# Kernel optimization log

Hardware: AMD Instinct MI355X
Metric: run time of the kernel (lower is better)

The kernel has to match this reference:

```python
import jax, jax.numpy as jnp
import numpy as np

# Dimensions matching init_kwargs
B, S, D, d_feat, O = 64, 1024, 64, 2, 10
L = S // 2  # label_site
STD = 0.01  # 'random_eye' init noise scale


def setup_inputs() -> dict:
    key = jax.random.key(0)
    k1, k2, k3, k4 = jax.random.split(key, 4)
    x = jax.random.normal(k1, (B, S, d_feat), dtype=jnp.float32)
    # InputRegion tensors, bond_str 'slri': eye over (l, r) broadcast over (s, i)
    W_left = jnp.eye(D, dtype=jnp.float32)[None, :, :, None] \
        + STD * jax.random.normal(k2, (L, D, D, d_feat), dtype=jnp.float32)
    W_right = jnp.eye(D, dtype=jnp.float32)[None, :, :, None] \
        + STD * jax.random.normal(k3, (S - L, D, D, d_feat), dtype=jnp.float32)
    # OutputSite tensor, bond_str 'olr': eye over (l, r) broadcast over o
    out_core = jnp.eye(D, dtype=jnp.float32)[None, :, :] \
        + STD * jax.random.normal(k4, (O, D, D), dtype=jnp.float32)
    return {"x": x, "W_left": W_left, "out_core": out_core, "W_right": W_right}


def reference(x, W_left, out_core, W_right):
    # x: [B, S, d]; W_left: [L, D, D, d]; out_core: [O, D, D]; W_right: [S-L, D, D, d]
    Ls = W_left.shape[0]
    Dv = W_left.shape[1]
    Bv = x.shape[0]
    # Per-site matrices (einsum 'slri,bsi->bslr'), laid out scan-major [S, B, D, D]
    mats_l = jnp.einsum('slri,bsi->sblr', W_left, x[:, :Ls])
    mats_r = jnp.einsum('slri,bsi->sblr', W_right, x[:, Ls:])
    # Open boundary edge vectors e = [1, 0, ..., 0]
    e = jnp.zeros((Dv,), dtype=x.dtype).at[0].set(1.0)
    v0 = jnp.broadcast_to(e, (Bv, Dv))
    # Left-to-right vector propagation through left chain
    def lstep(v, m):
        return jnp.einsum('bl,blr->br', v, m), None
    vL, _ = jax.lax.scan(lstep, v0, mats_l)
    # Right-to-left vector propagation through right chain
    def rstep(w, m):
        return jnp.einsum('blr,br->bl', m, w), None
    wR, _ = jax.lax.scan(rstep, v0, mats_r, reverse=True)
    # Contract through the output core: [B, O]
    return jnp.einsum('bl,olr,br->bo', vL, out_core, wR)
```

## Files before the change

### kernel.cpp

```cpp
#include <hip/hip_runtime.h>
#include <stdint.h>

#define NSITE 512
#define DD    64
#define NB    64
#define NO    10
#define NSEG  16
#define SEGLEN 32
#define SLAB_BYTES 32768
#define PACK_BYTES 16384

typedef short bf16x8 __attribute__((ext_vector_type(8)));
typedef float f32x16 __attribute__((ext_vector_type(16)));

__device__ __forceinline__ uint32_t pk2(float a, float b) {
    return __builtin_amdgcn_perm(__float_as_uint(b), __float_as_uint(a), 0x07060302);
}

__device__ __forceinline__ float2 pkmul2(float2 a, float2 b) {
    float2 r;
    asm("v_pk_mul_f32 %0, %1, %2" : "=v"(r) : "v"(a), "v"(b));
    return r;
}

__global__ __launch_bounds__(256) void pack_kernel(float* __restrict__ wl,
                                                   float* __restrict__ wr) {
    const int g = blockIdx.x;
    const int right = (g >= NSITE) ? 1 : 0;
    const int s = right ? g - NSITE : g;
    float* base = (right ? wr : wl) + (size_t)s * (SLAB_BYTES / 4);

    __shared__ float2 st[DD * 65];
    const float4* src4 = (const float4*)base;
    for (int e4 = threadIdx.x; e4 < DD * DD / 2; e4 += 256) {
        const float4 v = src4[e4];
        const int e = e4 * 2;
        float2* d = &st[(e >> 6) * 65 + (e & 63)];
        d[0] = make_float2(v.x, v.y);
        d[1] = make_float2(v.z, v.w);
    }
    __syncthreads();

    uint32_t* out = (uint32_t*)base;
    #pragma unroll
    for (int rr = 0; rr < 16; ++rr) {
        const int od = rr * 256 + threadIdx.x;
        const int chunk = od >> 8, i = chunk >> 3, sk = chunk & 7;
        const int H = (od >> 7) & 1, m5 = (od >> 2) & 31, d = od & 3;
        const int m = 32 * i + m5, k = 8 * sk + 4 * H + d;
        const float2 a = right ? st[m * 65 + k] : st[k * 65 + m];
        out[od] = pk2(a.x, a.y);
    }
}

__device__ __forceinline__ void dma16(const void* gp, void* lp) {
    __builtin_amdgcn_global_load_lds(
        (const __attribute__((address_space(1))) uint32_t*)gp,
        (__attribute__((address_space(3))) uint32_t*)lp, 16, 0, 0);
}

__global__ __launch_bounds__(256, 2) void stage1_kernel(
        const float* __restrict__ x, float* __restrict__ wl, float* __restrict__ wr) {
    const int bid  = blockIdx.x;
    const int side = bid >> 8;
    const int seg  = (bid >> 4) & 15;
    const int bq   = bid & 15;
    const int wave = threadIdx.x >> 6;
    const int lane = threadIdx.x & 63;
    const int b    = bq * 4 + wave;
    const int m5   = lane & 31;
    const int H    = lane >> 5;

    __shared__ __align__(16) char ring[4][PACK_BYTES];
    __shared__ float2 xs[4][SEGLEN];

    char* wbuf = (char*)(side ? wr : wl);

    if (lane < SEGLEN) {
        const float2* xp = ((const float2*)x) + (size_t)b * 1024 + (side ? NSITE : 0);
        const int sg = seg * SEGLEN + (side ? SEGLEN - 1 - lane : lane);
        xs[wave][lane] = xp[sg];
    }

    auto siteAddr = [&](int t) -> const char* {
        const int sg = seg * SEGLEN + (side ? SEGLEN - 1 - t : t);
        return wbuf + (size_t)sg * SLAB_BYTES;
    };

    #pragma unroll
    for (int t0 = 0; t0 < 2; ++t0) {
        const char* sb = siteAddr(t0);
        #pragma unroll
        for (int c = 0; c < 4; ++c) {
            const int ch = wave * 4 + c;
            dma16(sb + ch * 1024 + lane * 16, ring[t0] + ch * 1024);
        }
    }

    f32x16 acc[2][2];
    #pragma unroll
    for (int i = 0; i < 2; ++i)
        #pragma unroll
        for (int j = 0; j < 2; ++j)
            #pragma unroll
            for (int q = 0; q < 16; ++q) {
                const int row = (q & 3) + 8 * (q >> 2) + 4 * H;
                acc[i][j][q] = (i == j && row == m5) ? 1.f : 0.f;
            }

    f32x16 zf;
    #pragma unroll
    for (int q = 0; q < 16; ++q) zf[q] = 0.f;

    union BU { bf16x8 v; uint32_t w[4]; };

    for (int t = 0; t < SEGLEN; ++t) {
        int t2 = t + 2; if (t2 > SEGLEN - 1) t2 = SEGLEN - 1;
        {
            const char* sb = siteAddr(t2);
            char* lb = ring[(t + 2) & 3];
            #pragma unroll
            for (int c = 0; c < 4; ++c) {
                const int ch = wave * 4 + c;
                dma16(sb + ch * 1024 + lane * 16, lb + ch * 1024);
            }
        }
        asm volatile("s_waitcnt vmcnt(8)" ::: "memory");
        asm volatile("s_barrier" ::: "memory");

        const char* rb = ring[t & 3];
        const float2 xv = xs[wave][t];
        const float2 xx = make_float2(xv.x, xv.x);
        const float2 xy = make_float2(xv.y, xv.y);

        BU bfa[8][2];
        #pragma unroll
        for (int sk = 0; sk < 8; ++sk) {
            const int mi = sk >> 2, qb = 4 * (sk & 3);
            #pragma unroll
            for (int j = 0; j < 2; ++j)
                #pragma unroll
                for (int dp = 0; dp < 2; ++dp) {
                    const float2 v01 = make_float2(acc[mi][j][qb + 2 * dp],
                                                   acc[mi][j][qb + 2 * dp + 1]);
                    const float2 pa = pkmul2(xx, v01);
                    const float2 pb = pkmul2(xy, v01);
                    bfa[sk][j].w[2 * dp + 0] = pk2(pa.x, pb.x);
                    bfa[sk][j].w[2 * dp + 1] = pk2(pa.y, pb.y);
                }
        }

        __builtin_amdgcn_s_setprio(1);
        #pragma unroll
        for (int sk = 0; sk < 8; ++sk) {
            #pragma unroll
            for (int i = 0; i < 2; ++i) {
                union { bf16x8 v; uint4 u; } a;
                a.u = *(const uint4*)(rb + (i * 8 + sk) * 1024 + lane * 16);
                #pragma unroll
                for (int j = 0; j < 2; ++j)
                    acc[i][j] = __builtin_amdgcn_mfma_f32_32x32x16_bf16(
                        a.v, bfa[sk][j].v, (sk == 0) ? zf : acc[i][j], 0, 0, 0);
            }
        }
        __builtin_amdgcn_s_setprio(0);
    }

    {
        const int p = b * NSEG + seg;
        char* pdst = wbuf + (size_t)(p >> 1) * SLAB_BYTES + PACK_BYTES + (p & 1) * 8192;
        #pragma unroll
        for (int i = 0; i < 2; ++i)
            #pragma unroll
            for (int j = 0; j < 2; ++j) {
                const int c = 32 * j + m5;
                #pragma unroll
                for (int Q = 0; Q < 4; ++Q) {
                    const int r0 = 32 * i + 8 * Q + 4 * H;
                    uint2 val;
                    val.x = pk2(acc[i][j][4 * Q + 0], acc[i][j][4 * Q + 1]);
                    val.y = pk2(acc[i][j][4 * Q + 2], acc[i][j][4 * Q + 3]);
                    *(uint2*)(pdst + c * 128 + r0 * 2) = val;
                }
            }
    }
    asm volatile("s_waitcnt vmcnt(0)" ::: "memory");
}

__global__ __launch_bounds__(256) void stage2_kernel(
        const float* __restrict__ wl, const float* __restrict__ wr,
        float* __restrict__ vbuf) {
    const int chain = blockIdx.x;
    const int side  = chain >> 6, b = chain & 63;
    const int tid   = threadIdx.x, r = tid & 63, cg = tid >> 6;
    const char* wbuf = (const char*)(side ? wr : wl);

    __shared__ float vsh[DD];
    __shared__ float part[4][DD];
    if (tid < DD) vsh[tid] = (tid == 0) ? 1.f : 0.f;

    auto Pseg = [&](int gi) -> const uint16_t* {
        const int g = side ? (NSEG - 1 - gi) : gi;
        const int p = b * NSEG + g;
        return (const uint16_t*)(wbuf
            + (size_t)(p >> 1) * SLAB_BYTES + PACK_BYTES + (p & 1) * 8192);
    };

    float pv[16];
    {
        const uint16_t* P = Pseg(0);
        #pragma unroll
        for (int cc = 0; cc < 16; ++cc)
            pv[cc] = __uint_as_float(((uint32_t)P[(cg * 16 + cc) * 64 + r]) << 16);
    }
    __syncthreads();

    for (int gi = 0; gi < NSEG; ++gi) {
        float nv[16];
        const bool more = (gi + 1 < NSEG);
        if (more) {
            const uint16_t* Pn = Pseg(gi + 1);
            #pragma unroll
            for (int cc = 0; cc < 16; ++cc)
                nv[cc] = __uint_as_float(((uint32_t)Pn[(cg * 16 + cc) * 64 + r]) << 16);
        }
        float acc = 0.f;
        #pragma unroll
        for (int cc = 0; cc < 16; ++cc)
            acc = fmaf(vsh[cg * 16 + cc], pv[cc], acc);
        part[cg][r] = acc;
        asm volatile("s_waitcnt lgkmcnt(0)" ::: "memory");
        __builtin_amdgcn_s_barrier();
        if (tid < DD) vsh[tid] = part[0][tid] + part[1][tid] + part[2][tid] + part[3][tid];
        asm volatile("s_waitcnt lgkmcnt(0)" ::: "memory");
        __builtin_amdgcn_s_barrier();
        if (more) {
            #pragma unroll
            for (int cc = 0; cc < 16; ++cc) pv[cc] = nv[cc];
        }
    }
    if (tid < DD) vbuf[chain * DD + tid] = vsh[tid];
}

__global__ __launch_bounds__(64) void finalize_kernel(
        const float* __restrict__ core,
        const float* __restrict__ vbuf,
        float* __restrict__ out) {
    const int b    = blockIdx.x;
    const int lane = threadIdx.x;
    __shared__ float vls[DD];
    vls[lane] = vbuf[b * DD + lane];
    const float wr = vbuf[(NB + b) * DD + lane];
    __syncthreads();
    for (int o = 0; o < NO; ++o) {
        float acc = 0.f;
        #pragma unroll 8
        for (int l = 0; l < DD; ++l)
            acc += vls[l] * core[(o * DD + l) * DD + lane];
        acc *= wr;
        #pragma unroll
        for (int off = 32; off > 0; off >>= 1)
            acc += __shfl_xor(acc, off, 64);
        if (lane == 0) out[b * NO + o] = acc;
    }
}

extern "C" void kernel_launch(void* const* d_in, const int* in_sizes, int n_in,
                              void* d_out, int out_size, void* d_ws, size_t ws_size,
                              hipStream_t stream) {
    const float* x    = (const float*)d_in[0];
    float*       wl   = (float*)d_in[1];
    const float* core = (const float*)d_in[2];
    float*       wr   = (float*)d_in[3];
    float* vbuf = (float*)d_ws;

    pack_kernel<<<2 * NSITE, 256, 0, stream>>>(wl, wr);
    stage1_kernel<<<512, 256, 0, stream>>>(x, wl, wr);
    stage2_kernel<<<2 * NB, 256, 0, stream>>>(wl, wr, vbuf);
    finalize_kernel<<<NB, DD, 0, stream>>>(core, vbuf, (float*)d_out);
}
```

Baseline: 181.0 us.

## Fuse stage2 chains and finalize into one tail kernel; remap stage1 block order

Merges the left and right chain propagation for a batch element into one 512-thread block and performs the output-core contraction in the same block. This removes the finalize launch and the vbuf round trip through global memory. Stage1 block indices are also permuted to change how work is spread across CUs. The number of tail blocks is halved, so fewer CUs are used, and the barriers now synchronise both chains together.

Measured after the change: 166.6 us. 8.0% less time.

```diff
diff --git a/kernel.cpp b/kernel.cpp
--- a/kernel.cpp
+++ b/kernel.cpp
@@ -61,7 +61,8 @@
 
 __global__ __launch_bounds__(256, 2) void stage1_kernel(
         const float* __restrict__ x, float* __restrict__ wl, float* __restrict__ wr) {
-    const int bid  = blockIdx.x;
+    const int pb   = blockIdx.x;
+    const int bid  = (pb & 7) * 64 + (pb >> 3);
     const int side = bid >> 8;
     const int seg  = (bid >> 4) & 15;
     const int bq   = bid & 15;
@@ -187,17 +188,19 @@
     asm volatile("s_waitcnt vmcnt(0)" ::: "memory");
 }
 
-__global__ __launch_bounds__(256) void stage2_kernel(
+__global__ __launch_bounds__(512) void tail_kernel(
         const float* __restrict__ wl, const float* __restrict__ wr,
-        float* __restrict__ vbuf) {
-    const int chain = blockIdx.x;
-    const int side  = chain >> 6, b = chain & 63;
-    const int tid   = threadIdx.x, r = tid & 63, cg = tid >> 6;
+        const float* __restrict__ core, float* __restrict__ out) {
+    const int b    = blockIdx.x;
+    const int tid  = threadIdx.x;
+    const int side = tid >> 8;
+    const int r    = tid & 63;
+    const int cg   = (tid >> 6) & 3;
     const char* wbuf = (const char*)(side ? wr : wl);
 
-    __shared__ float vsh[DD];
-    __shared__ float part[4][DD];
-    if (tid < DD) vsh[tid] = (tid == 0) ? 1.f : 0.f;
+    __shared__ float vsh[2][DD];
+    __shared__ float part[2][4][DD];
+    if ((tid & 255) < DD) vsh[side][r] = (r == 0) ? 1.f : 0.f;
 
     auto Pseg = [&](int gi) -> const uint16_t* {
         const int g = side ? (NSEG - 1 - gi) : gi;
@@ -227,11 +230,13 @@
         float acc = 0.f;
         #pragma unroll
         for (int cc = 0; cc < 16; ++cc)
-            acc = fmaf(vsh[cg * 16 + cc], pv[cc], acc);
-        part[cg][r] = acc;
+            acc = fmaf(vsh[side][cg * 16 + cc], pv[cc], acc);
+        part[side][cg][r] = acc;
         asm volatile("s_waitcnt lgkmcnt(0)" ::: "memory");
         __builtin_amdgcn_s_barrier();
-        if (tid < DD) vsh[tid] = part[0][tid] + part[1][tid] + part[2][tid] + part[3][tid];
+        if ((tid & 255) < DD)
+            vsh[side][r] = part[side][0][r] + part[side][1][r]
+                         + part[side][2][r] + part[side][3][r];
         asm volatile("s_waitcnt lgkmcnt(0)" ::: "memory");
         __builtin_amdgcn_s_barrier();
         if (more) {
@@ -239,25 +244,15 @@
             for (int cc = 0; cc < 16; ++cc) pv[cc] = nv[cc];
         }
     }
-    if (tid < DD) vbuf[chain * DD + tid] = vsh[tid];
-}
-
-__global__ __launch_bounds__(64) void finalize_kernel(
-        const float* __restrict__ core,
-        const float* __restrict__ vbuf,
-        float* __restrict__ out) {
-    const int b    = blockIdx.x;
-    const int lane = threadIdx.x;
-    __shared__ float vls[DD];
-    vls[lane] = vbuf[b * DD + lane];
-    const float wr = vbuf[(NB + b) * DD + lane];
-    __syncthreads();
-    for (int o = 0; o < NO; ++o) {
+    const int wv   = tid >> 6;
+    const int lane = tid & 63;
+    const float wrv = vsh[1][lane];
+    for (int o = wv; o < NO; o += 8) {
         float acc = 0.f;
         #pragma unroll 8
         for (int l = 0; l < DD; ++l)
-            acc += vls[l] * core[(o * DD + l) * DD + lane];
-        acc *= wr;
+            acc += vsh[0][l] * core[(o * DD + l) * DD + lane];
+        acc *= wrv;
         #pragma unroll
         for (int off = 32; off > 0; off >>= 1)
             acc += __shfl_xor(acc, off, 64);
@@ -272,10 +267,8 @@
     float*       wl   = (float*)d_in[1];
     const float* core = (const float*)d_in[2];
     float*       wr   = (float*)d_in[3];
-    float* vbuf = (float*)d_ws;
 
     pack_kernel<<<2 * NSITE, 256, 0, stream>>>(wl, wr);
     stage1_kernel<<<512, 256, 0, stream>>>(x, wl, wr);
-    stage2_kernel<<<2 * NB, 256, 0, stream>>>(wl, wr, vbuf);
-    finalize_kernel<<<NB, DD, 0, stream>>>(core, vbuf, (float*)d_out);
-}
+    tail_kernel<<<NB, 512, 0, stream>>>(wl, wr, core, (float*)d_out);
+}
```
